# Kernel tuning notes

Measured on AMD Instinct MI355X. Metric: run time of the kernel, lower is better.

## Reference

```python
import jax, jax.numpy as jnp
import numpy as np

B, F, U, O, A, H = 8192, 1024, 512, 3, 6, 4  # batch, features, nb_units, nb_opponents, actions, heads
HD = U // H  # head dim


def setup_inputs() -> dict:
    key = jax.random.key(0)
    ks = jax.random.split(key, 12)
    s = 0.02
    rn = lambda k, shape: jax.random.normal(k, shape, jnp.float32) * s
    return {
        "features": jax.random.normal(ks[0], (B, F), jnp.float32),
        # agent latent Linear
        "W_al": rn(ks[1], (U, F)), "b_al": jnp.zeros((U,), jnp.float32),
        # MultiheadAttention in_proj (q,k,v stacked) and out_proj
        "W_in": rn(ks[2], (3 * U, U)), "b_in": jnp.zeros((3 * U,), jnp.float32),
        "W_out": rn(ks[3], (U, U)), "b_out": jnp.zeros((U,), jnp.float32),
        # agent head / policy / value
        "W_ah": rn(ks[4], (U, 2 * U)), "b_ah": jnp.zeros((U,), jnp.float32),
        "W_ap": rn(ks[5], (A, U)), "b_ap": jnp.zeros((A,), jnp.float32),
        "W_av": rn(ks[6], (1, U)), "b_av": jnp.zeros((1,), jnp.float32),
        # per-opponent stacks: latent, head, policy, value
        "W_ol": rn(ks[7], (O, U, F)), "b_ol": jnp.zeros((O, U), jnp.float32),
        "W_oh": rn(ks[8], (O, U, U)), "b_oh": jnp.zeros((O, U), jnp.float32),
        "W_op": rn(ks[9], (O, A, U)), "b_op": jnp.zeros((O, A), jnp.float32),
        "W_ov": rn(ks[10], (O, 1, U)), "b_ov": jnp.zeros((O, 1), jnp.float32),
    }


def reference(features, W_al, b_al, W_in, b_in, W_out, b_out, W_ah, b_ah,
              W_ap, b_ap, W_av, b_av, W_ol, b_ol, W_oh, b_oh, W_op, b_op, W_ov, b_ov):
    elu = jax.nn.elu
    # agent + per-opponent latents (per-opponent linears as one grouped GEMM)
    agent_latent = elu(features @ W_al.T + b_al)                                # [B,U]
    opp_lat = elu(jnp.einsum('bf,ouf->obu', features, W_ol) + b_ol[:, None, :])  # [O,B,U]

    # torch.nn.MultiheadAttention: query=[1,B,U] (agent), key=value=[O,B,U] (opponents)
    Wq, Wk, Wv = W_in[:U], W_in[U:2 * U], W_in[2 * U:]
    bq, bk, bv = b_in[:U], b_in[U:2 * U], b_in[2 * U:]
    q = (agent_latent @ Wq.T + bq).reshape(B, H, HD) * (1.0 / np.sqrt(HD))      # [B,H,HD]
    k = (jnp.einsum('obu,vu->obv', opp_lat, Wk) + bk).reshape(O, B, H, HD)
    v = (jnp.einsum('obu,vu->obv', opp_lat, Wv) + bv).reshape(O, B, H, HD)
    scores = jnp.einsum('bhd,obhd->bho', q, k)                                  # [B,H,O]
    w = jax.nn.softmax(scores, axis=-1)
    attn = jnp.einsum('bho,obhd->bhd', w, v).reshape(B, U)
    attn_out = attn @ W_out.T + b_out                                           # [B,U]
    opponents_influences = w.mean(axis=1)                                       # [B,O] (avg over heads)

    # agent head / policy / value
    cat = jnp.concatenate([agent_latent, attn_out], axis=1)                     # [B,2U]
    agent_head = elu(cat @ W_ah.T + b_ah)
    agent_policy = agent_head @ W_ap.T + b_ap                                   # [B,A]
    agent_value = agent_head @ W_av.T + b_av                                    # [B,1]

    # per-opponent head / policy / value (grouped GEMMs)
    opp_heads = elu(jnp.einsum('obu,ovu->obv', opp_lat, W_oh) + b_oh[:, None, :])  # [O,B,U]
    opponents_policies = jnp.einsum('obu,oau->boa', opp_heads, W_op) + b_op[None]   # [B,O,A]
    opponents_values = jnp.einsum('obu,ocu->boc', opp_heads, W_ov) + b_ov[None]     # [B,O,1]

    return (agent_policy, agent_value, opponents_policies, opponents_values, opponents_influences)
```

## Files before the change

kernel.cpp:

```cpp
#include <hip/hip_runtime.h>

typedef unsigned short u16;
typedef __bf16 bf16x8 __attribute__((ext_vector_type(8)));
typedef float f32x4 __attribute__((ext_vector_type(4)));

#define Bsz 8192
#define Fdim 1024
#define Udim 512
#define Odim 3
#define Adim 6
#define Hdim 4

#define OFF_FEAT   0
#define OFF_WAL    8388608
#define OFF_WOL    8912896
#define OFF_WIN    10485760
#define OFF_WOUT   11272192
#define OFF_WAH    11534336
#define OFF_WOH    12058624
#define OFF_LAT    12845056
#define OFF_Q      29622272
#define OFF_KV     33816576
#define OFF_ATT    58982400
#define OFF_AOUT   63176704
#define OFF_AGH    67371008
#define OFF_OPH    71565312

#define OUT_AP 0
#define OUT_AV 49152
#define OUT_OP 57344
#define OUT_OV 204800
#define OUT_IN 229376

__device__ __forceinline__ u16 f2bf(float f) {
  return __builtin_bit_cast(u16, (__bf16)f);
}
__device__ __forceinline__ float bf2f(u16 u) {
  return (float)__builtin_bit_cast(__bf16, u);
}

__device__ __forceinline__ void gload16(const u16* g, u16* s) {
  __builtin_amdgcn_global_load_lds(
      (const __attribute__((address_space(1))) unsigned int*)g,
      (__attribute__((address_space(3))) unsigned int*)s, 16, 0, 0);
}

#define CV_E0 2097152
#define CV_E1 2228224
#define CV_E2 2621440
#define CV_E3 2818048
#define CV_E4 2883584
#define CV_E5 3014656
#define CV_E6 3211264
__global__ __launch_bounds__(256) void convert_all(
    const float* __restrict__ f, const float* __restrict__ wal,
    const float* __restrict__ wol, const float* __restrict__ win,
    const float* __restrict__ wout, const float* __restrict__ wah,
    const float* __restrict__ woh, u16* __restrict__ dst) {
  int i = blockIdx.x * 256 + threadIdx.x;
  if (i >= CV_E6) return;
  const float* src;
  int base;
  if (i < CV_E0)      { src = f;    base = 0; }
  else if (i < CV_E1) { src = wal;  base = CV_E0; }
  else if (i < CV_E2) { src = wol;  base = CV_E1; }
  else if (i < CV_E3) { src = win;  base = CV_E2; }
  else if (i < CV_E4) { src = wout; base = CV_E3; }
  else if (i < CV_E5) { src = wah;  base = CV_E4; }
  else                { src = woh;  base = CV_E5; }
  float4 v = ((const float4*)src)[i - base];
  ushort4 o;
  o.x = f2bf(v.x); o.y = f2bf(v.y); o.z = f2bf(v.z); o.w = f2bf(v.w);
  ((ushort4*)dst)[i] = o;
}

#define BAR() __builtin_amdgcn_s_barrier()
#define FENCE() asm volatile("" ::: "memory")
#define LGKM0() asm volatile("s_waitcnt lgkmcnt(0)" ::: "memory")
#define VMW(n) asm volatile("s_waitcnt vmcnt(" #n ")" ::: "memory")
#define STAGE(MAT, SRC, LD, buf, ks, kb) do {                    \
    const u16* _s = (SRC) + (size_t)(kb) + (ks) * 32;            \
    gload16(_s, &MAT[buf][ks][wave * 512]);                      \
    gload16(_s + (size_t)128 * (LD), &MAT[buf][ks][4096 + wave * 512]); \
  } while (0)
#define RD_A(cur, ks, mh) do {                                   \
    _Pragma("unroll")                                            \
    for (int mi = 0; mi < 4; mi++)                               \
      a0[mi] = *(const bf16x8*)&As[cur][ks][aoff + (mh)*2048 + mi*512]; \
  } while (0)
#define RD_B(cur, ks) do {                                       \
    _Pragma("unroll")                                            \
    for (int ni = 0; ni < 4; ni++)                               \
      b0[ni] = *(const bf16x8*)&Bs[cur][ks][boff + ni*512];      \
  } while (0)
#define MFMA8(mh) do {                                           \
    __builtin_amdgcn_s_setprio(1);                               \
    _Pragma("unroll")                                            \
    for (int mi = 0; mi < 4; mi++) {                             \
      _Pragma("unroll")                                          \
      for (int ni = 0; ni < 4; ni++)                             \
        acc[(mh)*4+mi][ni] = __builtin_amdgcn_mfma_f32_16x16x32_bf16( \
            a0[mi], b0[ni], acc[(mh)*4+mi][ni], 0, 0, 0);        \
    }                                                            \
    __builtin_amdgcn_s_setprio(0);                               \
  } while (0)

template <bool ELU>
__global__ __launch_bounds__(512, 2) void gemm256(
    const u16* __restrict__ A, const u16* __restrict__ Bw, u16* __restrict__ C,
    const float* __restrict__ bias1, const float* __restrict__ bias2,
    int bsplit, int K, int lda, int ldb, int ldc,
    long sAz, long sBz, long sCz, int sbz, float scale) {
  __shared__ __align__(16) u16 As[2][2][8192];
  __shared__ __align__(16) u16 Bs[2][2][8192];
  const int tid = threadIdx.x;
  const int wave = tid >> 6, lane = tid & 63;
  const int wr = wave >> 2, wc = wave & 3;

  const int nx = gridDim.x, ny = gridDim.y;
  const int nxy = nx * ny;
  const int nwg = nxy * gridDim.z;
  const int orig = blockIdx.x + nx * (blockIdx.y + ny * blockIdx.z);
  const int xcd = orig & 7;
  const int qd = nwg >> 3, rd = nwg & 7;
  const int wg = (xcd < rd ? xcd * (qd + 1) : rd * (qd + 1) + (xcd - rd) * qd)
               + (orig >> 3);
  const int z = wg / nxy;
  const int rem = wg - z * nxy;
  const int by = rem / nx;
  const int bx = rem - by * nx;

  A += (size_t)z * sAz;
  Bw += (size_t)z * sBz;
  C += (size_t)z * sCz;
  bias1 += (size_t)z * sbz;

  const int tM = by * 256, tN = bx * 256;

  const int srow = tid >> 2;
  const int schunk = ((tid & 3) ^ ((tid >> 3) & 3)) * 8;
  const u16* Asrc = A + (size_t)(tM + srow) * lda + schunk;
  const u16* Bsrc = Bw + (size_t)(tN + srow) * ldb + schunk;

  const int laneLo = lane & 15;
  const int pc8 = (((lane >> 4) ^ ((lane >> 1) & 3))) * 8;
  const int aoff = (wr * 128 + laneLo) * 32 + pc8;
  const int boff = (wc * 64 + laneLo) * 32 + pc8;

  f32x4 acc[8][4];
#pragma unroll
  for (int mi = 0; mi < 8; mi++)
#pragma unroll
    for (int ni = 0; ni < 4; ni++) acc[mi][ni] = (f32x4){0.f, 0.f, 0.f, 0.f};

  const int NT = K >> 6;

  STAGE(As, Asrc, lda, 0, 0, 0);
  STAGE(Bs, Bsrc, ldb, 0, 0, 0);
  STAGE(As, Asrc, lda, 0, 1, 0);
  STAGE(Bs, Bsrc, ldb, 0, 1, 0);
  VMW(4);
  BAR();

  int cur = 0;
  int kb = 64;
  bf16x8 a0[4], b0[4];
  for (int t = 0; t < NT; ++t) {
    const int nxt = cur ^ 1;
    const bool st = (t + 1 < NT);
    RD_B(cur, 0);
    RD_A(cur, 0, 0);
    if (st) STAGE(As, Asrc, lda, nxt, 0, kb);
    FENCE(); BAR(); LGKM0();
    MFMA8(0);
    FENCE(); BAR();
    RD_A(cur, 0, 1);
    if (st) STAGE(Bs, Bsrc, ldb, nxt, 0, kb);
    FENCE(); BAR(); LGKM0();
    MFMA8(1);
    if (st) { VMW(4); } else { VMW(0); }
    BAR();
    RD_B(cur, 1);
    RD_A(cur, 1, 0);
    if (st) STAGE(As, Asrc, lda, nxt, 1, kb);
    FENCE(); BAR(); LGKM0();
    MFMA8(0);
    FENCE(); BAR();
    RD_A(cur, 1, 1);
    if (st) STAGE(Bs, Bsrc, ldb, nxt, 1, kb);
    FENCE(); BAR(); LGKM0();
    MFMA8(1);
    if (st) { VMW(4); BAR(); }
    cur = nxt;
    kb += 64;
  }

#pragma unroll
  for (int ni = 0; ni < 4; ni++) {
    const int col = tN + wc * 64 + ni * 16 + laneLo;
    const float bv = (col < bsplit) ? bias1[col] : bias2[col - bsplit];
#pragma unroll
    for (int gm = 0; gm < 8; gm++) {
      const int row0 = tM + wr * 128 + gm * 16 + (lane >> 4) * 4;
#pragma unroll
      for (int r = 0; r < 4; r++) {
        float v = (acc[gm][ni][r] + bv) * scale;
        if (ELU) v = v > 0.f ? v : (__expf(v) - 1.f);
        C[(size_t)(row0 + r) * ldc + col] = f2bf(v);
      }
    }
  }
}
#undef STAGE
#undef RD_A
#undef RD_B
#undef MFMA8

template <int BN, bool ELU>
__global__ __launch_bounds__(256) void gemm_bt(
    const u16* __restrict__ A, const u16* __restrict__ A2, int ksplit, int lda2,
    const u16* __restrict__ Bw, u16* __restrict__ C,
    const float* __restrict__ bias, int K, int lda, int ldb, int ldc,
    long sAz, long sBz, long sCz, int sbz, float scale) {
  constexpr int BM = 128, BK = 32;
  constexpr int NI = BN / 32;
  __shared__ __align__(16) u16 As[BM * BK];
  __shared__ __align__(16) u16 Bs[BN * BK];
  const int wave = threadIdx.x >> 6, lane = threadIdx.x & 63;

  const int nx = gridDim.x, ny = gridDim.y;
  const int nxy = nx * ny;
  const int nwg = nxy * gridDim.z;
  const int orig = blockIdx.x + nx * (blockIdx.y + ny * blockIdx.z);
  const int xcd = orig & 7;
  const int qd = nwg >> 3, rd = nwg & 7;
  const int wg = (xcd < rd ? xcd * (qd + 1) : rd * (qd + 1) + (xcd - rd) * qd)
               + (orig >> 3);
  const int z = wg / nxy;
  const int rem = wg - z * nxy;
  const int by = rem / nx;
  const int bx = rem - by * nx;

  A += (size_t)z * sAz;
  Bw += (size_t)z * sBz;
  C += (size_t)z * sCz;
  bias += (size_t)z * sbz;
  const int tM = by * BM, tN = bx * BN;
  const int wr = wave >> 1, wc = wave & 1;

  f32x4 acc[4][NI];
#pragma unroll
  for (int i = 0; i < 4; i++)
#pragma unroll
    for (int j = 0; j < NI; j++) acc[i][j] = (f32x4){0.f, 0.f, 0.f, 0.f};

  const int srow = lane >> 2;
  const int scol = (lane & 3) * 8;

  for (int k0 = 0; k0 < K; k0 += BK) {
    const u16* Ap;
    int la, kk;
    if (k0 < ksplit) { Ap = A;  la = lda;  kk = k0; }
    else             { Ap = A2; la = lda2; kk = k0 - ksplit; }
    __syncthreads();
#pragma unroll
    for (int i = 0; i < 2; ++i) {
      int r = wave * 32 + i * 16;
      gload16(Ap + (size_t)(tM + r + srow) * la + kk + scol, &As[r * BK]);
    }
#pragma unroll
    for (int i = 0; i < BN / 64; ++i) {
      int r = (wave * (BN / 64) + i) * 16;
      gload16(Bw + (size_t)(tN + r + srow) * ldb + k0 + scol, &Bs[r * BK]);
    }
    __syncthreads();
    bf16x8 af[4], bfr[NI];
#pragma unroll
    for (int mi = 0; mi < 4; mi++)
      af[mi] = *(const bf16x8*)&As[(wr * 64 + mi * 16 + (lane & 15)) * BK + (lane >> 4) * 8];
#pragma unroll
    for (int ni = 0; ni < NI; ni++)
      bfr[ni] = *(const bf16x8*)&Bs[(wc * (BN / 2) + ni * 16 + (lane & 15)) * BK + (lane >> 4) * 8];
#pragma unroll
    for (int mi = 0; mi < 4; mi++)
#pragma unroll
      for (int ni = 0; ni < NI; ni++)
        acc[mi][ni] = __builtin_amdgcn_mfma_f32_16x16x32_bf16(af[mi], bfr[ni], acc[mi][ni], 0, 0, 0);
  }

#pragma unroll
  for (int ni = 0; ni < NI; ni++) {
    int col = tN + wc * (BN / 2) + ni * 16 + (lane & 15);
    float bv = bias[col];
#pragma unroll
    for (int mi = 0; mi < 4; mi++) {
      int row0 = tM + wr * 64 + mi * 16 + (lane >> 4) * 4;
#pragma unroll
      for (int r = 0; r < 4; r++) {
        float v = (acc[mi][ni][r] + bv) * scale;
        if (ELU) v = v > 0.f ? v : (__expf(v) - 1.f);
        C[(size_t)(row0 + r) * ldc + col] = f2bf(v);
      }
    }
  }
}

__global__ __launch_bounds__(256) void attn_kernel(
    const u16* __restrict__ q, const u16* __restrict__ kv,
    u16* __restrict__ attn, float* __restrict__ influ) {
  const int wave = threadIdx.x >> 6, lane = threadIdx.x & 63;
  const int b = blockIdx.x * 4 + wave;
  const size_t qb = (size_t)b * 512;
  float wacc0 = 0.f, wacc1 = 0.f, wacc2 = 0.f;
#pragma unroll
  for (int h = 0; h < 4; ++h) {
    const int off = h * 128 + lane * 2;
    ushort2 qu = *(const ushort2*)(q + qb + off);
    float qx = bf2f(qu.x), qy = bf2f(qu.y);
    float s[3];
#pragma unroll
    for (int o = 0; o < 3; ++o) {
      ushort2 ku = *(const ushort2*)(kv + (size_t)o * (Bsz * 1024) + (size_t)b * 1024 + off);
      float p = qx * bf2f(ku.x) + qy * bf2f(ku.y);
#pragma unroll
      for (int d = 32; d; d >>= 1) p += __shfl_xor(p, d, 64);
      s[o] = p;
    }
    float m = fmaxf(s[0], fmaxf(s[1], s[2]));
    float e0 = __expf(s[0] - m), e1 = __expf(s[1] - m), e2 = __expf(s[2] - m);
    float inv = 1.f / (e0 + e1 + e2);
    float w0 = e0 * inv, w1 = e1 * inv, w2 = e2 * inv;
    wacc0 += w0; wacc1 += w1; wacc2 += w2;
    float ax = 0.f, ay = 0.f;
#pragma unroll
    for (int o = 0; o < 3; ++o) {
      float w = (o == 0) ? w0 : (o == 1) ? w1 : w2;
      ushort2 vu = *(const ushort2*)(kv + (size_t)o * (Bsz * 1024) + (size_t)b * 1024 + 512 + off);
      ax += w * bf2f(vu.x);
      ay += w * bf2f(vu.y);
    }
    ushort2 st; st.x = f2bf(ax); st.y = f2bf(ay);
    *(ushort2*)(attn + qb + off) = st;
  }
  if (lane == 0) {
    influ[b * 3 + 0] = wacc0 * 0.25f;
    influ[b * 3 + 1] = wacc1 * 0.25f;
    influ[b * 3 + 2] = wacc2 * 0.25f;
  }
}

__global__ __launch_bounds__(256) void heads_kernel(
    const u16* __restrict__ ah, const u16* __restrict__ oh,
    const float* __restrict__ Wap, const float* __restrict__ bap,
    const float* __restrict__ Wav, const float* __restrict__ bav,
    const float* __restrict__ Wop, const float* __restrict__ bop,
    const float* __restrict__ Wov, const float* __restrict__ bov,
    float* __restrict__ out) {
  __shared__ float sW[14336];
  for (int i = threadIdx.x; i < 14336; i += 256) {
    int s = i / 3584, rem = i - s * 3584;
    float v;
    if (s == 0) {
      v = (rem < 3072) ? Wap[rem] : Wav[rem - 3072];
    } else {
      int o = s - 1;
      v = (rem < 3072) ? Wop[o * 3072 + rem] : Wov[o * 512 + (rem - 3072)];
    }
    sW[i] = v;
  }
  __syncthreads();
  const int wave = threadIdx.x >> 6, lane = threadIdx.x & 63;
  const int kq = lane & 7, r = lane >> 3;
  const int b = blockIdx.x * 32 + wave * 8 + r;

  const u16* srcs[4] = {ah + (size_t)b * 512,
                        oh + (size_t)b * 512,
                        oh + (size_t)(Bsz + b) * 512,
                        oh + (size_t)(2 * Bsz + b) * 512};
  bf16x8 a[4][8];
#pragma unroll
  for (int s = 0; s < 4; s++)
#pragma unroll
    for (int c = 0; c < 8; c++)
      a[s][c] = *(const bf16x8*)(srcs[s] + c * 64 + kq * 8);

#pragma unroll
  for (int s = 0; s < 4; s++) {
#pragma unroll
    for (int p = 0; p < 7; p++) {
      const float* w = &sW[s * 3584 + p * 512 + kq * 8];
      float acc = 0.f;
#pragma unroll
      for (int c = 0; c < 8; c++) {
#pragma unroll
        for (int j = 0; j < 8; j++)
          acc += (float)a[s][c][j] * w[c * 64 + j];
      }
      acc += __shfl_xor(acc, 1, 64);
      acc += __shfl_xor(acc, 2, 64);
      acc += __shfl_xor(acc, 4, 64);
      if (kq == p) {
        if (s == 0) {
          if (p < 6) out[OUT_AP + b * 6 + p] = acc + bap[p];
          else       out[OUT_AV + b] = acc + bav[0];
        } else {
          int o = s - 1;
          if (p < 6) out[OUT_OP + b * 18 + o * 6 + p] = acc + bop[o * 6 + p];
          else       out[OUT_OV + b * 3 + o] = acc + bov[o];
        }
      }
    }
  }
}

extern "C" void kernel_launch(void* const* d_in, const int* in_sizes, int n_in,
                              void* d_out, int out_size, void* d_ws, size_t ws_size,
                              hipStream_t stream) {
  (void)in_sizes; (void)n_in; (void)out_size; (void)ws_size;
  const float* f     = (const float*)d_in[0];
  const float* W_al  = (const float*)d_in[1];
  const float* b_al  = (const float*)d_in[2];
  const float* W_in  = (const float*)d_in[3];
  const float* b_in  = (const float*)d_in[4];
  const float* W_out = (const float*)d_in[5];
  const float* b_out = (const float*)d_in[6];
  const float* W_ah  = (const float*)d_in[7];
  const float* b_ah  = (const float*)d_in[8];
  const float* W_ap  = (const float*)d_in[9];
  const float* b_ap  = (const float*)d_in[10];
  const float* W_av  = (const float*)d_in[11];
  const float* b_av  = (const float*)d_in[12];
  const float* W_ol  = (const float*)d_in[13];
  const float* b_ol  = (const float*)d_in[14];
  const float* W_oh  = (const float*)d_in[15];
  const float* b_oh  = (const float*)d_in[16];
  const float* W_op  = (const float*)d_in[17];
  const float* b_op  = (const float*)d_in[18];
  const float* W_ov  = (const float*)d_in[19];
  const float* b_ov  = (const float*)d_in[20];
  float* out = (float*)d_out;
  u16* ws = (u16*)d_ws;

  u16* feat = ws + OFF_FEAT;
  u16* wal  = ws + OFF_WAL;
  u16* win  = ws + OFF_WIN;
  u16* wout = ws + OFF_WOUT;
  u16* wah  = ws + OFF_WAH;
  u16* woh  = ws + OFF_WOH;
  u16* lat  = ws + OFF_LAT;
  u16* qb   = ws + OFF_Q;
  u16* kvb  = ws + OFF_KV;
  u16* att  = ws + OFF_ATT;
  u16* aout = ws + OFF_AOUT;
  u16* agh  = ws + OFF_AGH;
  u16* oph  = ws + OFF_OPH;

  convert_all<<<12544, 256, 0, stream>>>(f, W_al, W_ol, W_in, W_out, W_ah,
                                         W_oh, ws);

  gemm256<true><<<dim3(8, 32, 1), 512, 0, stream>>>(
      feat, wal, lat, b_al, b_ol, 512, 1024, 1024, 1024, 2048, 0, 0, 0, 0, 1.f);
  gemm_bt<64, false><<<dim3(8, 64, 1), 256, 0, stream>>>(
      lat, lat, 1 << 30, 2048, win, qb, b_in, 512, 2048, 512, 512,
      0, 0, 0, 0, 0.08838834764831845f);
  gemm256<false><<<dim3(4, 32, 3), 512, 0, stream>>>(
      lat + 512, win + 262144, kvb, b_in + 512, b_in + 512, 1 << 30,
      512, 2048, 512, 1024, 512, 0, 8388608, 0, 1.f);

  attn_kernel<<<2048, 256, 0, stream>>>(qb, kvb, att, out + OUT_IN);

  gemm_bt<64, false><<<dim3(8, 64, 1), 256, 0, stream>>>(
      att, att, 1 << 30, 512, wout, aout, b_out, 512, 512, 512, 512,
      0, 0, 0, 0, 1.f);
  gemm_bt<64, true><<<dim3(8, 64, 1), 256, 0, stream>>>(
      lat, aout, 512, 512, wah, agh, b_ah, 1024, 2048, 1024, 512,
      0, 0, 0, 0, 1.f);
  gemm_bt<128, true><<<dim3(4, 64, 3), 256, 0, stream>>>(
      lat + 512, lat + 512, 1 << 30, 2048, woh, oph, b_oh, 512, 2048, 512, 512,
      512, 262144, 4194304, 512, 1.f);

  heads_kernel<<<256, 256, 0, stream>>>(agh, oph, W_ap, b_ap, W_av, b_av,
                                        W_op, b_op, W_ov, b_ov, out);
}
```

Baseline: 324.6 us.

## Fuse attention, output projection, and all head stages into one per-row-tile kernel

Replaces the Q/KV projection GEMMs, the attention kernel, the out-projection, the agent-head and opponent-head GEMMs, and the heads kernel with a single kernel. Each block handles 32 batch rows, keeps the latents and intermediates in swizzled LDS, and reads weight fragments directly from global memory/L2. This removes several launches and the large round-trips of Q, K/V, attention and head intermediates through HBM. In exchange, every block re-streams all the weights through L2, and only one 512-thread block fits per CU because of the large LDS footprint, so the kernel may end up latency- or L2-bandwidth-bound.

```diff
diff --git a/kernel.cpp b/kernel.cpp
--- a/kernel.cpp
+++ b/kernel.cpp
@@ -19,12 +19,6 @@
 #define OFF_WAH    11534336
 #define OFF_WOH    12058624
 #define OFF_LAT    12845056
-#define OFF_Q      29622272
-#define OFF_KV     33816576
-#define OFF_ATT    58982400
-#define OFF_AOUT   63176704
-#define OFF_AGH    67371008
-#define OFF_OPH    71565312
 
 #define OUT_AP 0
 #define OUT_AV 49152
@@ -78,6 +72,7 @@
 #define FENCE() asm volatile("" ::: "memory")
 #define LGKM0() asm volatile("s_waitcnt lgkmcnt(0)" ::: "memory")
 #define VMW(n) asm volatile("s_waitcnt vmcnt(" #n ")" ::: "memory")
+#define MFMA(a, b, c) __builtin_amdgcn_mfma_f32_16x16x32_bf16(a, b, c, 0, 0, 0)
 #define STAGE(MAT, SRC, LD, buf, ks, kb) do {                    \
     const u16* _s = (SRC) + (size_t)(kb) + (ks) * 32;            \
     gload16(_s, &MAT[buf][ks][wave * 512]);                      \
@@ -99,8 +94,7 @@
     for (int mi = 0; mi < 4; mi++) {                             \
       _Pragma("unroll")                                          \
       for (int ni = 0; ni < 4; ni++)                             \
-        acc[(mh)*4+mi][ni] = __builtin_amdgcn_mfma_f32_16x16x32_bf16( \
-            a0[mi], b0[ni], acc[(mh)*4+mi][ni], 0, 0, 0);        \
+        acc[(mh)*4+mi][ni] = MFMA(a0[mi], b0[ni], acc[(mh)*4+mi][ni]); \
     }                                                            \
     __builtin_amdgcn_s_setprio(0);                               \
   } while (0)
@@ -216,200 +210,277 @@
 #undef RD_B
 #undef MFMA8
 
-template <int BN, bool ELU>
-__global__ __launch_bounds__(256) void gemm_bt(
-    const u16* __restrict__ A, const u16* __restrict__ A2, int ksplit, int lda2,
-    const u16* __restrict__ Bw, u16* __restrict__ C,
-    const float* __restrict__ bias, int K, int lda, int ldb, int ldc,
-    long sAz, long sBz, long sCz, int sbz, float scale) {
-  constexpr int BM = 128, BK = 32;
-  constexpr int NI = BN / 32;
-  __shared__ __align__(16) u16 As[BM * BK];
-  __shared__ __align__(16) u16 Bs[BN * BK];
-  const int wave = threadIdx.x >> 6, lane = threadIdx.x & 63;
-
-  const int nx = gridDim.x, ny = gridDim.y;
-  const int nxy = nx * ny;
-  const int nwg = nxy * gridDim.z;
-  const int orig = blockIdx.x + nx * (blockIdx.y + ny * blockIdx.z);
-  const int xcd = orig & 7;
-  const int qd = nwg >> 3, rd = nwg & 7;
-  const int wg = (xcd < rd ? xcd * (qd + 1) : rd * (qd + 1) + (xcd - rd) * qd)
-               + (orig >> 3);
-  const int z = wg / nxy;
-  const int rem = wg - z * nxy;
-  const int by = rem / nx;
-  const int bx = rem - by * nx;
-
-  A += (size_t)z * sAz;
-  Bw += (size_t)z * sBz;
-  C += (size_t)z * sCz;
-  bias += (size_t)z * sbz;
-  const int tM = by * BM, tN = bx * BN;
-  const int wr = wave >> 1, wc = wave & 1;
-
-  f32x4 acc[4][NI];
-#pragma unroll
-  for (int i = 0; i < 4; i++)
-#pragma unroll
-    for (int j = 0; j < NI; j++) acc[i][j] = (f32x4){0.f, 0.f, 0.f, 0.f};
-
-  const int srow = lane >> 2;
-  const int scol = (lane & 3) * 8;
-
-  for (int k0 = 0; k0 < K; k0 += BK) {
-    const u16* Ap;
-    int la, kk;
-    if (k0 < ksplit) { Ap = A;  la = lda;  kk = k0; }
-    else             { Ap = A2; la = lda2; kk = k0 - ksplit; }
-    __syncthreads();
-#pragma unroll
-    for (int i = 0; i < 2; ++i) {
-      int r = wave * 32 + i * 16;
-      gload16(Ap + (size_t)(tM + r + srow) * la + kk + scol, &As[r * BK]);
-    }
-#pragma unroll
-    for (int i = 0; i < BN / 64; ++i) {
-      int r = (wave * (BN / 64) + i) * 16;
-      gload16(Bw + (size_t)(tN + r + srow) * ldb + k0 + scol, &Bs[r * BK]);
-    }
-    __syncthreads();
-    bf16x8 af[4], bfr[NI];
-#pragma unroll
-    for (int mi = 0; mi < 4; mi++)
-      af[mi] = *(const bf16x8*)&As[(wr * 64 + mi * 16 + (lane & 15)) * BK + (lane >> 4) * 8];
-#pragma unroll
-    for (int ni = 0; ni < NI; ni++)
-      bfr[ni] = *(const bf16x8*)&Bs[(wc * (BN / 2) + ni * 16 + (lane & 15)) * BK + (lane >> 4) * 8];
-#pragma unroll
-    for (int mi = 0; mi < 4; mi++)
-#pragma unroll
-      for (int ni = 0; ni < NI; ni++)
-        acc[mi][ni] = __builtin_amdgcn_mfma_f32_16x16x32_bf16(af[mi], bfr[ni], acc[mi][ni], 0, 0, 0);
-  }
-
-#pragma unroll
-  for (int ni = 0; ni < NI; ni++) {
-    int col = tN + wc * (BN / 2) + ni * 16 + (lane & 15);
-    float bv = bias[col];
-#pragma unroll
-    for (int mi = 0; mi < 4; mi++) {
-      int row0 = tM + wr * 64 + mi * 16 + (lane >> 4) * 4;
-#pragma unroll
-      for (int r = 0; r < 4; r++) {
-        float v = (acc[mi][ni][r] + bv) * scale;
-        if (ELU) v = v > 0.f ? v : (__expf(v) - 1.f);
-        C[(size_t)(row0 + r) * ldc + col] = f2bf(v);
-      }
-    }
-  }
-}
-
-__global__ __launch_bounds__(256) void attn_kernel(
-    const u16* __restrict__ q, const u16* __restrict__ kv,
-    u16* __restrict__ attn, float* __restrict__ influ) {
-  const int wave = threadIdx.x >> 6, lane = threadIdx.x & 63;
-  const int b = blockIdx.x * 4 + wave;
-  const size_t qb = (size_t)b * 512;
-  float wacc0 = 0.f, wacc1 = 0.f, wacc2 = 0.f;
-#pragma unroll
-  for (int h = 0; h < 4; ++h) {
-    const int off = h * 128 + lane * 2;
-    ushort2 qu = *(const ushort2*)(q + qb + off);
-    float qx = bf2f(qu.x), qy = bf2f(qu.y);
-    float s[3];
-#pragma unroll
-    for (int o = 0; o < 3; ++o) {
-      ushort2 ku = *(const ushort2*)(kv + (size_t)o * (Bsz * 1024) + (size_t)b * 1024 + off);
-      float p = qx * bf2f(ku.x) + qy * bf2f(ku.y);
-#pragma unroll
-      for (int d = 32; d; d >>= 1) p += __shfl_xor(p, d, 64);
-      s[o] = p;
-    }
-    float m = fmaxf(s[0], fmaxf(s[1], s[2]));
-    float e0 = __expf(s[0] - m), e1 = __expf(s[1] - m), e2 = __expf(s[2] - m);
-    float inv = 1.f / (e0 + e1 + e2);
-    float w0 = e0 * inv, w1 = e1 * inv, w2 = e2 * inv;
-    wacc0 += w0; wacc1 += w1; wacc2 += w2;
-    float ax = 0.f, ay = 0.f;
-#pragma unroll
-    for (int o = 0; o < 3; ++o) {
-      float w = (o == 0) ? w0 : (o == 1) ? w1 : w2;
-      ushort2 vu = *(const ushort2*)(kv + (size_t)o * (Bsz * 1024) + (size_t)b * 1024 + 512 + off);
-      ax += w * bf2f(vu.x);
-      ay += w * bf2f(vu.y);
-    }
-    ushort2 st; st.x = f2bf(ax); st.y = f2bf(ay);
-    *(ushort2*)(attn + qb + off) = st;
-  }
-  if (lane == 0) {
-    influ[b * 3 + 0] = wacc0 * 0.25f;
-    influ[b * 3 + 1] = wacc1 * 0.25f;
-    influ[b * 3 + 2] = wacc2 * 0.25f;
-  }
-}
-
-__global__ __launch_bounds__(256) void heads_kernel(
-    const u16* __restrict__ ah, const u16* __restrict__ oh,
+#define GEMM16(ACC, BG, LDB, ABUF, AKB, BKB) do {                              \
+    _Pragma("unroll 4")                                                        \
+    for (int k_ = 0; k_ < 16; ++k_) {                                          \
+      bf16x8 af0_ = *(const bf16x8*)&(ABUF)[ll*512 + ((((AKB)+k_)*4+lh)^l7)*8];\
+      bf16x8 af1_ = *(const bf16x8*)&(ABUF)[(16+ll)*512 + ((((AKB)+k_)*4+lh)^l7)*8]; \
+      _Pragma("unroll")                                                        \
+      for (int nf_ = 0; nf_ < 4; ++nf_) {                                      \
+        bf16x8 bf_ = *(const bf16x8*)((BG) + (size_t)(wc0 + nf_*16 + ll)*(LDB) \
+                                      + ((BKB)+k_)*32 + lh*8);                 \
+        ACC[0][nf_] = MFMA(af0_, bf_, ACC[0][nf_]);                            \
+        ACC[1][nf_] = MFMA(af1_, bf_, ACC[1][nf_]);                            \
+      }                                                                        \
+    }                                                                          \
+  } while (0)
+
+#define ZACC(ACC) do {                                                         \
+    _Pragma("unroll")                                                          \
+    for (int mf_ = 0; mf_ < 2; ++mf_)                                          \
+      _Pragma("unroll")                                                        \
+      for (int nf_ = 0; nf_ < 4; ++nf_)                                        \
+        ACC[mf_][nf_] = (f32x4){0.f, 0.f, 0.f, 0.f};                           \
+  } while (0)
+
+#define STAGE_OL0(CB) do {                                                     \
+    _Pragma("unroll")                                                          \
+    for (int j_ = 0; j_ < 4; ++j_) {                                           \
+      int gq_ = j_*512 + tid;                                                  \
+      int r_ = gq_ >> 6, s_ = gq_ & 63, c_ = s_ ^ (r_ & 7);                    \
+      gload16(lat + (size_t)(row0 + r_)*2048 + (CB) + c_*8,                    \
+              &OL[0][j_*4096 + wave*512]);                                     \
+    }                                                                          \
+  } while (0)
+
+#define DOTS(BUF, WPp, BPp, WVp, BVp, AGENT, OO) do {                          \
+    if (wave < 4) {                                                            \
+      const int rl_ = wave*8 + (lane >> 3), kq_ = lane & 7;                    \
+      const int b_ = row0 + rl_;                                               \
+      bf16x8 av_[8];                                                           \
+      _Pragma("unroll")                                                        \
+      for (int c_ = 0; c_ < 8; ++c_)                                           \
+        av_[c_] = *(const bf16x8*)&(BUF)[rl_*512 + c_*64 + kq_*8];             \
+      _Pragma("unroll")                                                        \
+      for (int p_ = 0; p_ < 7; ++p_) {                                         \
+        const float* wg_ = (p_ < 6) ? (WPp) + p_*512 : (WVp);                  \
+        float ac_ = 0.f;                                                       \
+        _Pragma("unroll")                                                      \
+        for (int c_ = 0; c_ < 8; ++c_) {                                       \
+          float4 w0_ = *(const float4*)(wg_ + c_*64 + kq_*8);                  \
+          float4 w1_ = *(const float4*)(wg_ + c_*64 + kq_*8 + 4);              \
+          ac_ += (float)av_[c_][0]*w0_.x + (float)av_[c_][1]*w0_.y             \
+               + (float)av_[c_][2]*w0_.z + (float)av_[c_][3]*w0_.w             \
+               + (float)av_[c_][4]*w1_.x + (float)av_[c_][5]*w1_.y             \
+               + (float)av_[c_][6]*w1_.z + (float)av_[c_][7]*w1_.w;            \
+        }                                                                      \
+        ac_ += __shfl_xor(ac_, 1, 64);                                         \
+        ac_ += __shfl_xor(ac_, 2, 64);                                         \
+        ac_ += __shfl_xor(ac_, 4, 64);                                         \
+        if (kq_ == p_) {                                                       \
+          if (AGENT) {                                                         \
+            if (p_ < 6) out[OUT_AP + b_*6 + p_] = ac_ + (BPp)[p_];             \
+            else        out[OUT_AV + b_] = ac_ + (BVp)[0];                     \
+          } else {                                                             \
+            if (p_ < 6) out[OUT_OP + b_*18 + (OO)*6 + p_] = ac_ + (BPp)[(OO)*6 + p_]; \
+            else        out[OUT_OV + b_*3 + (OO)] = ac_ + (BVp)[(OO)];         \
+          }                                                                    \
+        }                                                                      \
+      }                                                                        \
+    }                                                                          \
+  } while (0)
+
+__global__ __launch_bounds__(512) void brain(
+    const u16* __restrict__ lat, const u16* __restrict__ win,
+    const u16* __restrict__ wout, const u16* __restrict__ wah,
+    const u16* __restrict__ woh,
+    const float* __restrict__ b_in, const float* __restrict__ b_out,
+    const float* __restrict__ b_ah, const float* __restrict__ b_oh,
     const float* __restrict__ Wap, const float* __restrict__ bap,
     const float* __restrict__ Wav, const float* __restrict__ bav,
     const float* __restrict__ Wop, const float* __restrict__ bop,
     const float* __restrict__ Wov, const float* __restrict__ bov,
     float* __restrict__ out) {
-  __shared__ float sW[14336];
-  for (int i = threadIdx.x; i < 14336; i += 256) {
-    int s = i / 3584, rem = i - s * 3584;
-    float v;
-    if (s == 0) {
-      v = (rem < 3072) ? Wap[rem] : Wav[rem - 3072];
-    } else {
-      int o = s - 1;
-      v = (rem < 3072) ? Wop[o * 3072 + rem] : Wov[o * 512 + (rem - 3072)];
-    }
-    sW[i] = v;
-  }
+  __shared__ __align__(16) u16 AL[16384];
+  __shared__ __align__(16) u16 OL[3][16384];
+  __shared__ float sc_s[2][384];
+  __shared__ float wt_s[384];
+
+  const int tid = threadIdx.x;
+  const int wave = tid >> 6, lane = tid & 63;
+  const int ll = lane & 15, lh = lane >> 4, l7 = lane & 7;
+  const int wc0 = wave * 64;
+  const int h3 = (wave >> 1) * 3;
+  const int wp = wave & 1;
+  const int row0 = blockIdx.x * 32;
+
+#pragma unroll
+  for (int j_ = 0; j_ < 4; ++j_) {
+    int gq_ = j_*512 + tid;
+    int r_ = gq_ >> 6, s_ = gq_ & 63, c_ = s_ ^ (r_ & 7);
+    const u16* src_ = lat + (size_t)(row0 + r_) * 2048 + c_ * 8;
+    gload16(src_,        &AL[j_*4096 + wave*512]);
+    gload16(src_ + 512,  &OL[0][j_*4096 + wave*512]);
+    gload16(src_ + 1024, &OL[1][j_*4096 + wave*512]);
+    gload16(src_ + 1536, &OL[2][j_*4096 + wave*512]);
+  }
+  for (int i = tid; i < 768; i += 512) ((float*)sc_s)[i] = 0.f;
   __syncthreads();
-  const int wave = threadIdx.x >> 6, lane = threadIdx.x & 63;
-  const int kq = lane & 7, r = lane >> 3;
-  const int b = blockIdx.x * 32 + wave * 8 + r;
-
-  const u16* srcs[4] = {ah + (size_t)b * 512,
-                        oh + (size_t)b * 512,
-                        oh + (size_t)(Bsz + b) * 512,
-                        oh + (size_t)(2 * Bsz + b) * 512};
-  bf16x8 a[4][8];
-#pragma unroll
-  for (int s = 0; s < 4; s++)
-#pragma unroll
-    for (int c = 0; c < 8; c++)
-      a[s][c] = *(const bf16x8*)(srcs[s] + c * 64 + kq * 8);
-
-#pragma unroll
-  for (int s = 0; s < 4; s++) {
-#pragma unroll
-    for (int p = 0; p < 7; p++) {
-      const float* w = &sW[s * 3584 + p * 512 + kq * 8];
-      float acc = 0.f;
-#pragma unroll
-      for (int c = 0; c < 8; c++) {
-#pragma unroll
-        for (int j = 0; j < 8; j++)
-          acc += (float)a[s][c][j] * w[c * 64 + j];
+
+  f32x4 qacc[2][4];
+  ZACC(qacc);
+  GEMM16(qacc, win, 512, AL, 0, 0);
+#pragma unroll
+  for (int nf = 0; nf < 4; ++nf) {
+    float bq_ = b_in[wc0 + nf*16 + ll];
+#pragma unroll
+    for (int mf = 0; mf < 2; ++mf)
+#pragma unroll
+      for (int rr = 0; rr < 4; ++rr)
+        qacc[mf][nf][rr] = (qacc[mf][nf][rr] + bq_) * 0.08838834764831845f;
+  }
+
+  float bkv[4];
+#pragma unroll
+  for (int nf = 0; nf < 4; ++nf) bkv[nf] = b_in[512 + wc0 + nf*16 + ll];
+  for (int o = 0; o < 3; ++o) {
+    f32x4 kacc[2][4];
+    ZACC(kacc);
+    GEMM16(kacc, win + 262144, 512, OL[o], 0, 0);
+    float part0[4] = {0.f, 0.f, 0.f, 0.f}, part1[4] = {0.f, 0.f, 0.f, 0.f};
+#pragma unroll
+    for (int nf = 0; nf < 4; ++nf)
+#pragma unroll
+      for (int rr = 0; rr < 4; ++rr) {
+        part0[rr] += qacc[0][nf][rr] * (kacc[0][nf][rr] + bkv[nf]);
+        part1[rr] += qacc[1][nf][rr] * (kacc[1][nf][rr] + bkv[nf]);
       }
-      acc += __shfl_xor(acc, 1, 64);
-      acc += __shfl_xor(acc, 2, 64);
-      acc += __shfl_xor(acc, 4, 64);
-      if (kq == p) {
-        if (s == 0) {
-          if (p < 6) out[OUT_AP + b * 6 + p] = acc + bap[p];
-          else       out[OUT_AV + b] = acc + bav[0];
-        } else {
-          int o = s - 1;
-          if (p < 6) out[OUT_OP + b * 18 + o * 6 + p] = acc + bop[o * 6 + p];
-          else       out[OUT_OV + b * 3 + o] = acc + bov[o];
-        }
+#pragma unroll
+    for (int rr = 0; rr < 4; ++rr) {
+      float p0 = part0[rr], p1 = part1[rr];
+      p0 += __shfl_xor(p0, 1, 64); p1 += __shfl_xor(p1, 1, 64);
+      p0 += __shfl_xor(p0, 2, 64); p1 += __shfl_xor(p1, 2, 64);
+      p0 += __shfl_xor(p0, 4, 64); p1 += __shfl_xor(p1, 4, 64);
+      p0 += __shfl_xor(p0, 8, 64); p1 += __shfl_xor(p1, 8, 64);
+      if (ll == 0) {
+        sc_s[wp][(lh*4 + rr)*12 + h3 + o] = p0;
+        sc_s[wp][(16 + lh*4 + rr)*12 + h3 + o] = p1;
       }
     }
+  }
+  __syncthreads();
+
+  if (tid < 128) {
+    int r = tid >> 2, h = tid & 3;
+    int i = r*12 + h*3;
+    float s0 = sc_s[0][i+0] + sc_s[1][i+0];
+    float s1 = sc_s[0][i+1] + sc_s[1][i+1];
+    float s2 = sc_s[0][i+2] + sc_s[1][i+2];
+    float m = fmaxf(s0, fmaxf(s1, s2));
+    float e0 = __expf(s0 - m), e1 = __expf(s1 - m), e2 = __expf(s2 - m);
+    float inv = 1.f / (e0 + e1 + e2);
+    wt_s[i+0] = e0 * inv; wt_s[i+1] = e1 * inv; wt_s[i+2] = e2 * inv;
+  }
+  __syncthreads();
+
+  if (tid < 96) {
+    int r = tid / 3, o = tid - r * 3;
+    out[OUT_IN + (size_t)(row0 + r)*3 + o] =
+        (wt_s[r*12 + o] + wt_s[r*12 + 3 + o] + wt_s[r*12 + 6 + o] +
+         wt_s[r*12 + 9 + o]) * 0.25f;
+  }
+
+  float bvv[4];
+#pragma unroll
+  for (int nf = 0; nf < 4; ++nf) bvv[nf] = b_in[1024 + wc0 + nf*16 + ll];
+  f32x4 att[2][4];
+  ZACC(att);
+  for (int o = 0; o < 3; ++o) {
+    f32x4 vacc[2][4];
+    ZACC(vacc);
+    GEMM16(vacc, win + 524288, 512, OL[o], 0, 0);
+#pragma unroll
+    for (int mf = 0; mf < 2; ++mf)
+#pragma unroll
+      for (int rr = 0; rr < 4; ++rr) {
+        float wv = wt_s[(mf*16 + lh*4 + rr)*12 + h3 + o];
+#pragma unroll
+        for (int nf = 0; nf < 4; ++nf)
+          att[mf][nf][rr] += wv * (vacc[mf][nf][rr] + bvv[nf]);
+      }
+  }
+#pragma unroll
+  for (int mf = 0; mf < 2; ++mf)
+#pragma unroll
+    for (int nf = 0; nf < 4; ++nf)
+#pragma unroll
+      for (int rr = 0; rr < 4; ++rr) {
+        int row = mf*16 + lh*4 + rr;
+        int col = wc0 + nf*16 + ll;
+        OL[1][row*512 + (((col >> 3) ^ (row & 7))*8) + (col & 7)] =
+            f2bf(att[mf][nf][rr]);
+      }
+  __syncthreads();
+
+  {
+    f32x4 ao[2][4];
+    ZACC(ao);
+    GEMM16(ao, wout, 512, OL[1], 0, 0);
+#pragma unroll
+    for (int nf = 0; nf < 4; ++nf) {
+      float bb = b_out[wc0 + nf*16 + ll];
+#pragma unroll
+      for (int mf = 0; mf < 2; ++mf)
+#pragma unroll
+        for (int rr = 0; rr < 4; ++rr) {
+          int row = mf*16 + lh*4 + rr;
+          int col = wc0 + nf*16 + ll;
+          OL[2][row*512 + (((col >> 3) ^ (row & 7))*8) + (col & 7)] =
+              f2bf(ao[mf][nf][rr] + bb);
+        }
+    }
+  }
+  __syncthreads();
+
+  {
+    f32x4 gh[2][4];
+    ZACC(gh);
+    GEMM16(gh, wah, 1024, AL, 0, 0);
+    GEMM16(gh, wah, 1024, OL[2], 0, 16);
+#pragma unroll
+    for (int nf = 0; nf < 4; ++nf) {
+      float bb = b_ah[wc0 + nf*16 + ll];
+#pragma unroll
+      for (int mf = 0; mf < 2; ++mf)
+#pragma unroll
+        for (int rr = 0; rr < 4; ++rr) {
+          int row = mf*16 + lh*4 + rr;
+          int col = wc0 + nf*16 + ll;
+          float v = gh[mf][nf][rr] + bb;
+          v = v > 0.f ? v : (__expf(v) - 1.f);
+          OL[1][row*512 + col] = f2bf(v);
+        }
+    }
+  }
+  __syncthreads();
+
+  DOTS(OL[1], Wap, bap, Wav, bav, 1, 0);
+
+  for (int o = 0; o < 3; ++o) {
+    if (o > 0) {
+      STAGE_OL0(512 * (1 + o));
+      __syncthreads();
+    }
+    const int dst = (o == 1) ? 1 : 2;
+    f32x4 oh[2][4];
+    ZACC(oh);
+    GEMM16(oh, woh + (size_t)o * 262144, 512, OL[0], 0, 0);
+#pragma unroll
+    for (int nf = 0; nf < 4; ++nf) {
+      float bb = b_oh[o*512 + wc0 + nf*16 + ll];
+#pragma unroll
+      for (int mf = 0; mf < 2; ++mf)
+#pragma unroll
+        for (int rr = 0; rr < 4; ++rr) {
+          int row = mf*16 + lh*4 + rr;
+          int col = wc0 + nf*16 + ll;
+          float v = oh[mf][nf][rr] + bb;
+          v = v > 0.f ? v : (__expf(v) - 1.f);
+          OL[dst][row*512 + col] = f2bf(v);
+        }
+    }
+    __syncthreads();
+    DOTS(OL[dst], Wop + (size_t)o * 3072, bop, Wov + (size_t)o * 512, bov, 0, o);
   }
 }
 
@@ -448,37 +519,15 @@
   u16* wah  = ws + OFF_WAH;
   u16* woh  = ws + OFF_WOH;
   u16* lat  = ws + OFF_LAT;
-  u16* qb   = ws + OFF_Q;
-  u16* kvb  = ws + OFF_KV;
-  u16* att  = ws + OFF_ATT;
-  u16* aout = ws + OFF_AOUT;
-  u16* agh  = ws + OFF_AGH;
-  u16* oph  = ws + OFF_OPH;
 
   convert_all<<<12544, 256, 0, stream>>>(f, W_al, W_ol, W_in, W_out, W_ah,
                                          W_oh, ws);
 
   gemm256<true><<<dim3(8, 32, 1), 512, 0, stream>>>(
       feat, wal, lat, b_al, b_ol, 512, 1024, 1024, 1024, 2048, 0, 0, 0, 0, 1.f);
-  gemm_bt<64, false><<<dim3(8, 64, 1), 256, 0, stream>>>(
-      lat, lat, 1 << 30, 2048, win, qb, b_in, 512, 2048, 512, 512,
-      0, 0, 0, 0, 0.08838834764831845f);
-  gemm256<false><<<dim3(4, 32, 3), 512, 0, stream>>>(
-      lat + 512, win + 262144, kvb, b_in + 512, b_in + 512, 1 << 30,
-      512, 2048, 512, 1024, 512, 0, 8388608, 0, 1.f);
-
-  attn_kernel<<<2048, 256, 0, stream>>>(qb, kvb, att, out + OUT_IN);
-
-  gemm_bt<64, false><<<dim3(8, 64, 1), 256, 0, stream>>>(
-      att, att, 1 << 30, 512, wout, aout, b_out, 512, 512, 512, 512,
-      0, 0, 0, 0, 1.f);
-  gemm_bt<64, true><<<dim3(8, 64, 1), 256, 0, stream>>>(
-      lat, aout, 512, 512, wah, agh, b_ah, 1024, 2048, 1024, 512,
-      0, 0, 0, 0, 1.f);
-  gemm_bt<128, true><<<dim3(4, 64, 3), 256, 0, stream>>>(
-      lat + 512, lat + 512, 1 << 30, 2048, woh, oph, b_oh, 512, 2048, 512, 512,
-      512, 262144, 4194304, 512, 1.f);
-
-  heads_kernel<<<256, 256, 0, stream>>>(agh, oph, W_ap, b_ap, W_av, b_av,
-                                        W_op, b_op, W_ov, b_ov, out);
-}
+
+  brain<<<256, 512, 0, stream>>>(lat, win, wout, wah, woh,
+                                 b_in, b_out, b_ah, b_oh,
+                                 W_ap, b_ap, W_av, b_av,
+                                 W_op, b_op, W_ov, b_ov, out);
+}
```

Result: slower. 384.4 us (+18.4%).

## Fold out-projection into agent head weights and merge independent GEMMs into one launch

Applied to the files above, without the earlier changes.

Precomputes W_ah[:,U:]·W_out as a combined weight, with the matching bias fold, so the attention output feeds the agent-head GEMM directly. This removes the separate out-projection GEMM and its intermediate buffer. The Q, KV, opponent-head and weight-combination GEMMs now run together in one multi-z 'mega' kernel, which cuts launches and improves occupancy. The cost is a small prep kernel with a serial bias dot-product, a weight product computed again on every call, extra rounding from the bf16 combined weight, and grid blocks that exit early in the mega launch.

```diff
diff --git a/kernel.cpp b/kernel.cpp
--- a/kernel.cpp
+++ b/kernel.cpp
@@ -13,7 +13,6 @@
 
 #define OFF_FEAT   0
 #define OFF_WAL    8388608
-#define OFF_WOL    8912896
 #define OFF_WIN    10485760
 #define OFF_WOUT   11272192
 #define OFF_WAH    11534336
@@ -22,9 +21,12 @@
 #define OFF_Q      29622272
 #define OFF_KV     33816576
 #define OFF_ATT    58982400
-#define OFF_AOUT   63176704
-#define OFF_AGH    67371008
-#define OFF_OPH    71565312
+#define OFF_AGH    63176704
+#define OFF_OPH    67371008
+#define OFF_WOUTT  79953920
+#define OFF_WCOMB  80216064
+#define OFF_BAHC   80478208
+#define OFF_ZB     80479232
 
 #define OUT_AP 0
 #define OUT_AV 49152
@@ -74,10 +76,44 @@
   ((ushort4*)dst)[i] = o;
 }
 
+__global__ __launch_bounds__(256) void prep(
+    const float* __restrict__ wout_f, const float* __restrict__ wah_f,
+    const float* __restrict__ bout_f, const float* __restrict__ bah_f,
+    u16* __restrict__ woutT, float* __restrict__ bahc, float* __restrict__ zb) {
+  if (blockIdx.x == 64) {
+    int t = threadIdx.x;
+    zb[t] = 0.f; zb[t + 256] = 0.f;
+    for (int j = t; j < 512; j += 256) {
+      float s = 0.f;
+      for (int v = 0; v < 512; ++v)
+        s += wah_f[j * 1024 + 512 + v] * bout_f[v];
+      bahc[j] = bah_f[j] + s;
+    }
+    return;
+  }
+  __shared__ float tile[64][65];
+  const int bx = blockIdx.x & 7, byy = blockIdx.x >> 3;
+  const int v0 = byy * 64, u0 = bx * 64;
+#pragma unroll
+  for (int it = 0; it < 16; ++it) {
+    int idx = it * 256 + threadIdx.x;
+    int r = idx >> 6, c = idx & 63;
+    tile[r][c] = wout_f[(v0 + r) * 512 + u0 + c];
+  }
+  __syncthreads();
+#pragma unroll
+  for (int it = 0; it < 16; ++it) {
+    int idx = it * 256 + threadIdx.x;
+    int r = idx >> 6, c = idx & 63;
+    woutT[(u0 + r) * 512 + v0 + c] = f2bf(tile[c][r]);
+  }
+}
+
 #define BAR() __builtin_amdgcn_s_barrier()
 #define FENCE() asm volatile("" ::: "memory")
 #define LGKM0() asm volatile("s_waitcnt lgkmcnt(0)" ::: "memory")
 #define VMW(n) asm volatile("s_waitcnt vmcnt(" #n ")" ::: "memory")
+#define MFMA(a, b, c) __builtin_amdgcn_mfma_f32_16x16x32_bf16(a, b, c, 0, 0, 0)
 #define STAGE(MAT, SRC, LD, buf, ks, kb) do {                    \
     const u16* _s = (SRC) + (size_t)(kb) + (ks) * 32;            \
     gload16(_s, &MAT[buf][ks][wave * 512]);                      \
@@ -99,8 +135,7 @@
     for (int mi = 0; mi < 4; mi++) {                             \
       _Pragma("unroll")                                          \
       for (int ni = 0; ni < 4; ni++)                             \
-        acc[(mh)*4+mi][ni] = __builtin_amdgcn_mfma_f32_16x16x32_bf16( \
-            a0[mi], b0[ni], acc[(mh)*4+mi][ni], 0, 0, 0);        \
+        acc[(mh)*4+mi][ni] = MFMA(a0[mi], b0[ni], acc[(mh)*4+mi][ni]); \
     }                                                            \
     __builtin_amdgcn_s_setprio(0);                               \
   } while (0)
@@ -218,12 +253,94 @@
 
 template <int BN, bool ELU>
 __global__ __launch_bounds__(256) void gemm_bt(
-    const u16* __restrict__ A, const u16* __restrict__ A2, int ksplit, int lda2,
-    const u16* __restrict__ Bw, u16* __restrict__ C,
-    const float* __restrict__ bias, int K, int lda, int ldb, int ldc,
-    long sAz, long sBz, long sCz, int sbz, float scale) {
+    const u16* __restrict__ A, const u16* __restrict__ A2,
+    const u16* __restrict__ Bw, const u16* __restrict__ Bw2,
+    int ksplit, int lda, int lda2, int ldb, int ldb2,
+    u16* __restrict__ C, const float* __restrict__ bias,
+    int K, int ldc, float scale) {
   constexpr int BM = 128, BK = 32;
   constexpr int NI = BN / 32;
+  __shared__ __align__(16) u16 As[BM * BK];
+  __shared__ __align__(16) u16 Bs[BN * BK];
+  const int wave = threadIdx.x >> 6, lane = threadIdx.x & 63;
+
+  const int nx = gridDim.x;
+  const int nwg = nx * gridDim.y;
+  const int orig = blockIdx.x + nx * blockIdx.y;
+  const int xcd = orig & 7;
+  const int qd = nwg >> 3, rd = nwg & 7;
+  const int wg = (xcd < rd ? xcd * (qd + 1) : rd * (qd + 1) + (xcd - rd) * qd)
+               + (orig >> 3);
+  const int by = wg / nx, bx = wg - by * nx;
+  const int tM = by * BM, tN = bx * BN;
+  const int wr = wave >> 1, wc = wave & 1;
+
+  f32x4 acc[4][NI];
+#pragma unroll
+  for (int i = 0; i < 4; i++)
+#pragma unroll
+    for (int j = 0; j < NI; j++) acc[i][j] = (f32x4){0.f, 0.f, 0.f, 0.f};
+
+  const int srow = lane >> 2;
+  const int scol = (lane & 3) * 8;
+
+  for (int k0 = 0; k0 < K; k0 += BK) {
+    const u16 *Ap, *Bp;
+    int la, lb, kk;
+    if (k0 < ksplit) { Ap = A;  la = lda;  Bp = Bw;  lb = ldb;  kk = k0; }
+    else             { Ap = A2; la = lda2; Bp = Bw2; lb = ldb2; kk = k0 - ksplit; }
+    __syncthreads();
+#pragma unroll
+    for (int i = 0; i < 2; ++i) {
+      int r = wave * 32 + i * 16;
+      gload16(Ap + (size_t)(tM + r + srow) * la + kk + scol, &As[r * BK]);
+    }
+#pragma unroll
+    for (int i = 0; i < BN / 64; ++i) {
+      int r = (wave * (BN / 64) + i) * 16;
+      gload16(Bp + (size_t)(tN + r + srow) * lb + kk + scol, &Bs[r * BK]);
+    }
+    __syncthreads();
+    bf16x8 af[4], bfr[NI];
+#pragma unroll
+    for (int mi = 0; mi < 4; mi++)
+      af[mi] = *(const bf16x8*)&As[(wr * 64 + mi * 16 + (lane & 15)) * BK + (lane >> 4) * 8];
+#pragma unroll
+    for (int ni = 0; ni < NI; ni++)
+      bfr[ni] = *(const bf16x8*)&Bs[(wc * (BN / 2) + ni * 16 + (lane & 15)) * BK + (lane >> 4) * 8];
+#pragma unroll
+    for (int mi = 0; mi < 4; mi++)
+#pragma unroll
+      for (int ni = 0; ni < NI; ni++)
+        acc[mi][ni] = __builtin_amdgcn_mfma_f32_16x16x32_bf16(af[mi], bfr[ni], acc[mi][ni], 0, 0, 0);
+  }
+
+#pragma unroll
+  for (int ni = 0; ni < NI; ni++) {
+    int col = tN + wc * (BN / 2) + ni * 16 + (lane & 15);
+    float bv = bias[col];
+#pragma unroll
+    for (int mi = 0; mi < 4; mi++) {
+      int row0 = tM + wr * 64 + mi * 16 + (lane >> 4) * 4;
+#pragma unroll
+      for (int r = 0; r < 4; r++) {
+        float v = (acc[mi][ni][r] + bv) * scale;
+        if (ELU) v = v > 0.f ? v : (__expf(v) - 1.f);
+        C[(size_t)(row0 + r) * ldc + col] = f2bf(v);
+      }
+    }
+  }
+}
+
+__global__ __launch_bounds__(256) void mega(
+    const u16* __restrict__ lat, const u16* __restrict__ win,
+    const u16* __restrict__ woh, const u16* __restrict__ wahb,
+    const u16* __restrict__ woutT,
+    u16* __restrict__ qb, u16* __restrict__ kvb, u16* __restrict__ oph,
+    u16* __restrict__ wcomb,
+    const float* __restrict__ b_in, const float* __restrict__ b_oh,
+    const float* __restrict__ zb) {
+  constexpr int BM = 128, BK = 32, BN = 128, NI = 4;
   __shared__ __align__(16) u16 As[BM * BK];
   __shared__ __align__(16) u16 Bs[BN * BK];
   const int wave = threadIdx.x >> 6, lane = threadIdx.x & 63;
@@ -241,11 +358,30 @@
   const int by = rem / nx;
   const int bx = rem - by * nx;
 
-  A += (size_t)z * sAz;
-  Bw += (size_t)z * sBz;
-  C += (size_t)z * sCz;
-  bias += (size_t)z * sbz;
+  const u16 *A, *Bw;
+  u16* C;
+  const float* bias;
+  int N, ldc, M = 8192, lda = 2048;
+  bool elu = false;
+  float scale = 1.f;
+  if (z == 0) {
+    A = lat; Bw = win; C = qb; bias = b_in;
+    N = 512; ldc = 512; scale = 0.08838834764831845f;
+  } else if (z <= 3) {
+    A = lat + 512 * z; Bw = win + 262144;
+    C = kvb + (size_t)(z - 1) * 8388608; bias = b_in + 512;
+    N = 1024; ldc = 1024;
+  } else if (z <= 6) {
+    A = lat + 512 * (z - 3); Bw = woh + (size_t)(z - 4) * 262144;
+    C = oph + (size_t)(z - 4) * 4194304; bias = b_oh + (z - 4) * 512;
+    N = 512; ldc = 512; elu = true;
+  } else {
+    A = wahb + 512; lda = 1024; Bw = woutT;
+    C = wcomb; bias = zb;
+    N = 512; ldc = 512; M = 512;
+  }
   const int tM = by * BM, tN = bx * BN;
+  if (tN >= N || tM >= M) return;
   const int wr = wave >> 1, wc = wave & 1;
 
   f32x4 acc[4][NI];
@@ -257,21 +393,17 @@
   const int srow = lane >> 2;
   const int scol = (lane & 3) * 8;
 
-  for (int k0 = 0; k0 < K; k0 += BK) {
-    const u16* Ap;
-    int la, kk;
-    if (k0 < ksplit) { Ap = A;  la = lda;  kk = k0; }
-    else             { Ap = A2; la = lda2; kk = k0 - ksplit; }
+  for (int k0 = 0; k0 < 512; k0 += BK) {
     __syncthreads();
 #pragma unroll
     for (int i = 0; i < 2; ++i) {
       int r = wave * 32 + i * 16;
-      gload16(Ap + (size_t)(tM + r + srow) * la + kk + scol, &As[r * BK]);
-    }
-#pragma unroll
-    for (int i = 0; i < BN / 64; ++i) {
-      int r = (wave * (BN / 64) + i) * 16;
-      gload16(Bw + (size_t)(tN + r + srow) * ldb + k0 + scol, &Bs[r * BK]);
+      gload16(A + (size_t)(tM + r + srow) * lda + k0 + scol, &As[r * BK]);
+    }
+#pragma unroll
+    for (int i = 0; i < 2; ++i) {
+      int r = (wave * 2 + i) * 16;
+      gload16(Bw + (size_t)(tN + r + srow) * 512 + k0 + scol, &Bs[r * BK]);
     }
     __syncthreads();
     bf16x8 af[4], bfr[NI];
@@ -280,7 +412,7 @@
       af[mi] = *(const bf16x8*)&As[(wr * 64 + mi * 16 + (lane & 15)) * BK + (lane >> 4) * 8];
 #pragma unroll
     for (int ni = 0; ni < NI; ni++)
-      bfr[ni] = *(const bf16x8*)&Bs[(wc * (BN / 2) + ni * 16 + (lane & 15)) * BK + (lane >> 4) * 8];
+      bfr[ni] = *(const bf16x8*)&Bs[(wc * 64 + ni * 16 + (lane & 15)) * BK + (lane >> 4) * 8];
 #pragma unroll
     for (int mi = 0; mi < 4; mi++)
 #pragma unroll
@@ -290,7 +422,7 @@
 
 #pragma unroll
   for (int ni = 0; ni < NI; ni++) {
-    int col = tN + wc * (BN / 2) + ni * 16 + (lane & 15);
+    int col = tN + wc * 64 + ni * 16 + (lane & 15);
     float bv = bias[col];
 #pragma unroll
     for (int mi = 0; mi < 4; mi++) {
@@ -298,7 +430,7 @@
 #pragma unroll
       for (int r = 0; r < 4; r++) {
         float v = (acc[mi][ni][r] + bv) * scale;
-        if (ELU) v = v > 0.f ? v : (__expf(v) - 1.f);
+        if (elu) v = v > 0.f ? v : (__expf(v) - 1.f);
         C[(size_t)(row0 + r) * ldc + col] = f2bf(v);
       }
     }
@@ -441,43 +573,37 @@
   float* out = (float*)d_out;
   u16* ws = (u16*)d_ws;
 
-  u16* feat = ws + OFF_FEAT;
-  u16* wal  = ws + OFF_WAL;
-  u16* win  = ws + OFF_WIN;
-  u16* wout = ws + OFF_WOUT;
-  u16* wah  = ws + OFF_WAH;
-  u16* woh  = ws + OFF_WOH;
-  u16* lat  = ws + OFF_LAT;
-  u16* qb   = ws + OFF_Q;
-  u16* kvb  = ws + OFF_KV;
-  u16* att  = ws + OFF_ATT;
-  u16* aout = ws + OFF_AOUT;
-  u16* agh  = ws + OFF_AGH;
-  u16* oph  = ws + OFF_OPH;
+  u16* feat  = ws + OFF_FEAT;
+  u16* wal   = ws + OFF_WAL;
+  u16* win   = ws + OFF_WIN;
+  u16* wahb  = ws + OFF_WAH;
+  u16* woh   = ws + OFF_WOH;
+  u16* lat   = ws + OFF_LAT;
+  u16* qb    = ws + OFF_Q;
+  u16* kvb   = ws + OFF_KV;
+  u16* att   = ws + OFF_ATT;
+  u16* agh   = ws + OFF_AGH;
+  u16* oph   = ws + OFF_OPH;
+  u16* woutT = ws + OFF_WOUTT;
+  u16* wcomb = ws + OFF_WCOMB;
+  float* bahc = (float*)(ws + OFF_BAHC);
+  float* zb   = (float*)(ws + OFF_ZB);
 
   convert_all<<<12544, 256, 0, stream>>>(f, W_al, W_ol, W_in, W_out, W_ah,
                                          W_oh, ws);
+  prep<<<65, 256, 0, stream>>>(W_out, W_ah, b_out, b_ah, woutT, bahc, zb);
 
   gemm256<true><<<dim3(8, 32, 1), 512, 0, stream>>>(
       feat, wal, lat, b_al, b_ol, 512, 1024, 1024, 1024, 2048, 0, 0, 0, 0, 1.f);
-  gemm_bt<64, false><<<dim3(8, 64, 1), 256, 0, stream>>>(
-      lat, lat, 1 << 30, 2048, win, qb, b_in, 512, 2048, 512, 512,
-      0, 0, 0, 0, 0.08838834764831845f);
-  gemm256<false><<<dim3(4, 32, 3), 512, 0, stream>>>(
-      lat + 512, win + 262144, kvb, b_in + 512, b_in + 512, 1 << 30,
-      512, 2048, 512, 1024, 512, 0, 8388608, 0, 1.f);
+
+  mega<<<dim3(8, 64, 8), 256, 0, stream>>>(
+      lat, win, woh, wahb, woutT, qb, kvb, oph, wcomb, b_in, b_oh, zb);
 
   attn_kernel<<<2048, 256, 0, stream>>>(qb, kvb, att, out + OUT_IN);
 
-  gemm_bt<64, false><<<dim3(8, 64, 1), 256, 0, stream>>>(
-      att, att, 1 << 30, 512, wout, aout, b_out, 512, 512, 512, 512,
-      0, 0, 0, 0, 1.f);
-  gemm_bt<64, true><<<dim3(8, 64, 1), 256, 0, stream>>>(
-      lat, aout, 512, 512, wah, agh, b_ah, 1024, 2048, 1024, 512,
-      0, 0, 0, 0, 1.f);
-  gemm_bt<128, true><<<dim3(4, 64, 3), 256, 0, stream>>>(
-      lat + 512, lat + 512, 1 << 30, 2048, woh, oph, b_oh, 512, 2048, 512, 512,
-      512, 262144, 4194304, 512, 1.f);
+  gemm_bt<64, true><<<dim3(8, 64), 256, 0, stream>>>(
+      lat, att, wahb, wcomb, 512, 2048, 512, 1024, 512,
+      agh, bahc, 1024, 512, 1.f);
 
   heads_kernel<<<256, 256, 0, stream>>>(agh, oph, W_ap, b_ap, W_av, b_av,
                                         W_op, b_op, W_ov, b_ov, out);
```

New measurement: 363.0 us. 11.8% more time.
